# Kernel tuning notes

Hardware: AMD Instinct MI355X
Metric: run time of the kernel (lower is better)

## Reference

```python
import jax, jax.numpy as jnp
import numpy as np

B, S, E, H = 4, 1024, 256, 12  # batch, seq, emb_dim, num_heads; per-head dim == E (module quirk)


def setup_inputs() -> dict:
    key = jax.random.key(0)
    ks = jax.random.split(key, 9)
    s = 0.02
    x = jax.random.normal(ks[0], (B, S, E), dtype=jnp.float32)
    # additive causal mask (the module's tril buffer is unused; mask arrives via attention_mask)
    causal = jnp.tril(jnp.ones((S, S), dtype=jnp.float32))
    attention_mask = ((1.0 - causal) * -10000.0)[None, None, :, :]
    Wq = jax.random.normal(ks[1], (E, E * H), dtype=jnp.float32) * s
    bq = jnp.zeros((E * H,), dtype=jnp.float32)
    Wk = jax.random.normal(ks[2], (E, E * H), dtype=jnp.float32) * s
    bk = jnp.zeros((E * H,), dtype=jnp.float32)
    Wv = jax.random.normal(ks[3], (E, E * H), dtype=jnp.float32) * s
    bv = jnp.zeros((E * H,), dtype=jnp.float32)
    Wfc = jax.random.normal(ks[4], (E * H, E), dtype=jnp.float32) * s
    bfc = jnp.zeros((E,), dtype=jnp.float32)
    return {"x": x, "attention_mask": attention_mask, "Wq": Wq, "bq": bq,
            "Wk": Wk, "bk": bk, "Wv": Wv, "bv": bv, "Wfc": Wfc, "bfc": bfc}


def _split_heads(t):
    # (B, S, H*E) -> (B, H, S, E)
    b, s, _ = t.shape
    return t.reshape(b, s, H, E).transpose(0, 2, 1, 3)


def reference(x, attention_mask, Wq, bq, Wk, bk, Wv, bv, Wfc, bfc):
    q = _split_heads(x @ Wq + bq)
    k = _split_heads(x @ Wk + bk)
    v = _split_heads(x @ Wv + bv)
    scale = 1.0 / jnp.sqrt(jnp.asarray(E, dtype=x.dtype))
    scores = jnp.einsum('bhqd,bhkd->bhqk', q, k) * scale + attention_mask
    probs = jax.nn.softmax(scores, axis=-1)  # dropout p=0 in eval reference
    ctx = jnp.einsum('bhqk,bhkd->bhqd', probs, v)
    merged = ctx.transpose(0, 2, 1, 3).reshape(x.shape[0], x.shape[1], H * E)
    return merged @ Wfc + bfc
```

## Files before the change

### kernel.cpp

```cpp
#include <hip/hip_runtime.h>

#define BATCH 4
#define SEQ   1024
#define EMB   256
#define NH    12
#define EH    3072
#define MROWS 4096

typedef __attribute__((ext_vector_type(8))) short bf16x8;
typedef __attribute__((ext_vector_type(4))) float f32x4;
typedef __attribute__((ext_vector_type(4))) short short4v;

__device__ __forceinline__ short f2bf(float f) {
  union { float f; unsigned u; } x; x.f = f;
  unsigned r = x.u + 0x7fffu + ((x.u >> 16) & 1u);
  return (short)(r >> 16);
}

__device__ __forceinline__ unsigned pack_trunc(float a, float b) {
  union { float f; unsigned u; } x, y;
  x.f = a; y.f = b;
  return (x.u >> 16) | (y.u & 0xffff0000u);
}

__device__ __forceinline__ void gload_lds16(const void* g, void* l) {
  __builtin_amdgcn_global_load_lds(
      (const __attribute__((address_space(1))) unsigned*)g,
      (__attribute__((address_space(3))) unsigned*)l, 16, 0, 0);
}

__global__ __launch_bounds__(256) void cast_x_kernel(const float* __restrict__ in,
                                                     short* __restrict__ out) {
  int i = (blockIdx.x * 256 + threadIdx.x) * 4;
  float4 v = *(const float4*)(in + i);
  short4v o;
  o[0] = f2bf(v.x); o[1] = f2bf(v.y); o[2] = f2bf(v.z); o[3] = f2bf(v.w);
  *(short4v*)(out + i) = o;
}

__global__ __launch_bounds__(256) void transpose_qkv_kernel(const float* __restrict__ Wq,
                                                            const float* __restrict__ Wk,
                                                            const float* __restrict__ Wv,
                                                            short* __restrict__ Wt) {
  __shared__ float tile[32][33];
  const float* W = blockIdx.z == 0 ? Wq : (blockIdx.z == 1 ? Wk : Wv);
  short* o = Wt + (size_t)blockIdx.z * EH * EMB;
  const int n0 = blockIdx.x * 32, k0 = blockIdx.y * 32;
  const int tx = threadIdx.x & 31, ty = threadIdx.x >> 5;
#pragma unroll
  for (int i = 0; i < 4; i++)
    tile[ty + 8 * i][tx] = W[(size_t)(k0 + ty + 8 * i) * EH + n0 + tx];
  __syncthreads();
#pragma unroll
  for (int i = 0; i < 4; i++) {
    int nr = ty + 8 * i;
    o[(size_t)(n0 + nr) * EMB + k0 + tx] = f2bf(tile[tx][nr]);
  }
}

__global__ __launch_bounds__(256) void transpose_cast_kernel(const float* __restrict__ W,
                                                             short* __restrict__ Wt,
                                                             int K, int N) {
  __shared__ float tile[32][33];
  const int n0 = blockIdx.x * 32, k0 = blockIdx.y * 32;
  const int tx = threadIdx.x & 31, ty = threadIdx.x >> 5;
#pragma unroll
  for (int i = 0; i < 4; i++)
    tile[ty + 8 * i][tx] = W[(size_t)(k0 + ty + 8 * i) * N + n0 + tx];
  __syncthreads();
#pragma unroll
  for (int i = 0; i < 4; i++) {
    int nr = ty + 8 * i;
    Wt[(size_t)(n0 + nr) * K + k0 + tx] = f2bf(tile[tx][nr]);
  }
}

__global__ __launch_bounds__(256) void qkv_gemm_kernel(const short* __restrict__ A,
                                                       const short* __restrict__ Bt,
                                                       const float* __restrict__ bq,
                                                       const float* __restrict__ bk,
                                                       const float* __restrict__ bv,
                                                       short* __restrict__ qout,
                                                       short* __restrict__ kout,
                                                       short* __restrict__ vout) {
  constexpr int BM = 128, BK = 64, K = EMB;
  __shared__ short As[2][BM * BK];
  __shared__ short Bs[2][BM * BK];
  const int tid = threadIdx.x;
  const int w = tid >> 6, lane = tid & 63;
  const int wm = w >> 1, wn = w & 1;
  const int l15 = lane & 15, l4 = lane >> 4;
  const int m0 = blockIdx.x * BM, n0 = blockIdx.y * BM;

  f32x4 acc[4][4] = {};

  int srow[4], scol[4];
#pragma unroll
  for (int i = 0; i < 4; i++) {
    const int idx = i * 256 + tid;
    const int row = idx >> 3, sp = idx & 7, sl = sp ^ (row & 7);
    srow[i] = row;
    scol[i] = sl * 8;
  }

#define QKV_STAGE(bu, k0)                                                        \
  {                                                                              \
    _Pragma("unroll") for (int i = 0; i < 4; i++) {                              \
      const int idx = i * 256 + tid;                                             \
      gload_lds16(A + (size_t)(m0 + srow[i]) * K + (k0) + scol[i],               \
                  (char*)&As[bu][0] + idx * 16);                                 \
      gload_lds16(Bt + (size_t)(n0 + srow[i]) * K + (k0) + scol[i],              \
                  (char*)&Bs[bu][0] + idx * 16);                                 \
    }                                                                            \
  }

  QKV_STAGE(0, 0);
  asm volatile("s_waitcnt vmcnt(0)" ::: "memory");
  __syncthreads();

  int bu = 0;
  for (int k0 = 0; k0 < K; k0 += BK) {
    if (k0 + BK < K) QKV_STAGE(bu ^ 1, k0 + BK);

#pragma unroll
    for (int kst = 0; kst < 2; kst++) {
      const int sp = (kst * 4 + l4) ^ (l15 & 7);
      bf16x8 af[4], bfr[4];
#pragma unroll
      for (int mt = 0; mt < 4; mt++)
        af[mt] = *(const bf16x8*)&As[bu][(wm * 64 + mt * 16 + l15) * 64 + sp * 8];
#pragma unroll
      for (int nt = 0; nt < 4; nt++)
        bfr[nt] = *(const bf16x8*)&Bs[bu][(wn * 64 + nt * 16 + l15) * 64 + sp * 8];
      __builtin_amdgcn_s_setprio(1);
#pragma unroll
      for (int mt = 0; mt < 4; mt++)
#pragma unroll
        for (int nt = 0; nt < 4; nt++)
          acc[mt][nt] = __builtin_amdgcn_mfma_f32_16x16x32_bf16(af[mt], bfr[nt], acc[mt][nt], 0, 0, 0);
      __builtin_amdgcn_s_setprio(0);
    }

    asm volatile("s_waitcnt vmcnt(0)" ::: "memory");
    __syncthreads();
    bu ^= 1;
  }

  const int region = n0 / 3072;
  const float* bias = region == 0 ? bq : (region == 1 ? bk : bv);
  const float kQScale = 0.09016844f;
#pragma unroll
  for (int nt = 0; nt < 4; nt++) {
    const int n = n0 + wn * 64 + nt * 16 + l15;
    const int col = n - region * 3072;
    const float bvv = bias[col];
#pragma unroll
    for (int mt = 0; mt < 4; mt++) {
      const int mrow = m0 + wm * 64 + mt * 16 + 4 * l4;
      f32x4 v = acc[mt][nt];
      if (region == 0) {
#pragma unroll
        for (int r = 0; r < 4; r++)
          qout[(size_t)(mrow + r) * EH + col] = f2bf((v[r] + bvv) * kQScale);
      } else if (region == 1) {
#pragma unroll
        for (int r = 0; r < 4; r++)
          kout[(size_t)(mrow + r) * EH + col] = f2bf(v[r] + bvv);
      } else {
        const int bb = mrow >> 10;
        const int s  = mrow & 1023;
        const int h  = col >> 8, d = col & 255;
        short4v o4;
        o4[0] = f2bf(v[0] + bvv); o4[1] = f2bf(v[1] + bvv);
        o4[2] = f2bf(v[2] + bvv); o4[3] = f2bf(v[3] + bvv);
        *(short4v*)&vout[((size_t)(bb * NH + h) * EMB + d) * SEQ + s] = o4;
      }
    }
  }
#undef QKV_STAGE
}

__global__ __launch_bounds__(256) void fc_partial_kernel(const short* __restrict__ A,
                                                         const short* __restrict__ Bt,
                                                         float* __restrict__ Pout,
                                                         int M, int N, int K) {
  constexpr int BM = 64, BK = 128, KSL = 768;
  __shared__ short As[2][BM * BK];
  __shared__ short Bs[2][BM * BK];
  const int tid = threadIdx.x;
  const int w = tid >> 6, lane = tid & 63;
  const int wm = w >> 1, wn = w & 1;
  const int l15 = lane & 15, l4 = lane >> 4;
  const int m0 = blockIdx.x * BM, n0 = blockIdx.y * BM;
  const int kbase = blockIdx.z * KSL;
  float* P = Pout + (size_t)blockIdx.z * M * N;

  f32x4 acc[2][2] = {};

  int srow[4], scol[4];
#pragma unroll
  for (int i = 0; i < 4; i++) {
    const int idx = i * 256 + tid;
    const int row = idx >> 4, sp = idx & 15, sl = sp ^ (row & 15);
    srow[i] = row;
    scol[i] = sl * 8;
  }

#define FC_STAGE(bu, k0)                                                         \
  {                                                                              \
    _Pragma("unroll") for (int i = 0; i < 4; i++) {                              \
      const int idx = i * 256 + tid;                                             \
      gload_lds16(A + (size_t)(m0 + srow[i]) * K + (k0) + scol[i],               \
                  (char*)&As[bu][0] + idx * 16);                                 \
      gload_lds16(Bt + (size_t)(n0 + srow[i]) * K + (k0) + scol[i],              \
                  (char*)&Bs[bu][0] + idx * 16);                                 \
    }                                                                            \
  }

  FC_STAGE(0, kbase);
  asm volatile("s_waitcnt vmcnt(0)" ::: "memory");
  __syncthreads();

  int bu = 0;
  for (int k0 = kbase; k0 < kbase + KSL; k0 += BK) {
    if (k0 + BK < kbase + KSL) FC_STAGE(bu ^ 1, k0 + BK);

#pragma unroll
    for (int kst = 0; kst < 4; kst++) {
      const int sp = (kst * 4 + l4) ^ l15;
      bf16x8 af[2], bfr[2];
#pragma unroll
      for (int mt = 0; mt < 2; mt++)
        af[mt] = *(const bf16x8*)&As[bu][(wm * 32 + mt * 16 + l15) * 128 + sp * 8];
#pragma unroll
      for (int nt = 0; nt < 2; nt++)
        bfr[nt] = *(const bf16x8*)&Bs[bu][(wn * 32 + nt * 16 + l15) * 128 + sp * 8];
      __builtin_amdgcn_s_setprio(1);
#pragma unroll
      for (int mt = 0; mt < 2; mt++)
#pragma unroll
        for (int nt = 0; nt < 2; nt++)
          acc[mt][nt] = __builtin_amdgcn_mfma_f32_16x16x32_bf16(af[mt], bfr[nt], acc[mt][nt], 0, 0, 0);
      __builtin_amdgcn_s_setprio(0);
    }

    asm volatile("s_waitcnt vmcnt(0)" ::: "memory");
    __syncthreads();
    bu ^= 1;
  }

#pragma unroll
  for (int nt = 0; nt < 2; nt++) {
    const int n = n0 + wn * 32 + nt * 16 + l15;
#pragma unroll
    for (int mt = 0; mt < 2; mt++) {
      const int mrow = m0 + wm * 32 + mt * 16 + 4 * l4;
      f32x4 v = acc[mt][nt];
#pragma unroll
      for (int r = 0; r < 4; r++)
        P[(size_t)(mrow + r) * N + n] = v[r];
    }
  }
#undef FC_STAGE
}

__global__ __launch_bounds__(256) void fc_reduce_kernel(const float* __restrict__ Pin,
                                                        const float* __restrict__ bias,
                                                        float* __restrict__ out) {
  const int i4 = (blockIdx.x * 256 + threadIdx.x) * 4;
  const int n = i4 & 255;
  float4 s = *(const float4*)(bias + n);
#pragma unroll
  for (int ks = 0; ks < 4; ks++) {
    float4 p = *(const float4*)(Pin + (size_t)ks * MROWS * EMB + i4);
    s.x += p.x; s.y += p.y; s.z += p.z; s.w += p.w;
  }
  *(float4*)(out + i4) = s;
}

__global__ __launch_bounds__(512) void attn_kernel(const short* __restrict__ Q,
                                                   const short* __restrict__ Kg,
                                                   const short* __restrict__ Vt,
                                                   short* __restrict__ Ctx) {
  __shared__ short Ks[2][8192];
  __shared__ short Vs[2][8192];
  __shared__ short Ps[8][512];
  const int tid = threadIdx.x, w = tid >> 6, lane = tid & 63;
  const int l15 = lane & 15, l4 = lane >> 4;
  const int bh = blockIdx.x, b = bh / NH, h = bh % NH;
  const int qt = (gridDim.y - 1) - blockIdx.y;
  const int q0 = qt * 128;
  const int qw0 = q0 + w * 16;
  const int ntiles = 4 * qt + 4;

  const float kMaskL2 = -14426.95f;
  const float kThrL2  = 11.5f;

  const short* Kbase = Kg + (size_t)b * SEQ * EH + h * EMB;
  const short* Vbase = Vt + (size_t)bh * EMB * SEQ;

  int koff[2], voff[2];
#pragma unroll
  for (int i = 0; i < 2; i++) {
    const int idx = i * 512 + tid;
    {
      const int kv = (idx >> 3) & 31, sp = idx & 7, sl = sp ^ (kv & 7);
      koff[i] = kv * EH + (idx >> 8) * 64 + sl * 8;
    }
    {
      const int dp = idx >> 3, sp = idx & 7, sl = sp ^ (dp & 7);
      voff[i] = (dp * 2 + (sl >> 2)) * SEQ + (sl & 3) * 8;
    }
  }

  bf16x8 qf[8];
  {
    const short* qp = Q + (size_t)(b * SEQ + qw0 + l15) * EH + h * EMB + 8 * l4;
#pragma unroll
    for (int kst = 0; kst < 8; kst++) qf[kst] = *(const bf16x8*)(qp + 32 * kst);
  }

#pragma unroll
  for (int i = 0; i < 2; i++) {
    const int idx = i * 512 + tid;
    gload_lds16(Kbase + koff[i], (char*)&Ks[0][0] + idx * 16);
    gload_lds16(Vbase + voff[i], (char*)&Vs[0][0] + idx * 16);
  }
  asm volatile("s_waitcnt vmcnt(0)" ::: "memory");
  __syncthreads();

  f32x4 o[16] = {};
  float mst = -1e30f, lst = 0.f;

  int bu = 0;
  for (int t = 0; t < ntiles; t++) {
    const int kv0 = t * 32;

    if (t + 1 < ntiles) {
      const short* kp = Kbase + (size_t)(kv0 + 32) * EH;
      const short* vp = Vbase + kv0 + 32;
#pragma unroll
      for (int i = 0; i < 2; i++) {
        const int idx = i * 512 + tid;
        gload_lds16(kp + koff[i], (char*)&Ks[bu ^ 1][0] + idx * 16);
        gload_lds16(vp + voff[i], (char*)&Vs[bu ^ 1][0] + idx * 16);
      }
    }

    if (kv0 <= qw0 + 15) {
      f32x4 sf[2] = {};
      __builtin_amdgcn_s_setprio(1);
#pragma unroll
      for (int nt = 0; nt < 2; nt++)
#pragma unroll
        for (int kst = 0; kst < 8; kst++) {
          const int sp = (((kst & 1) << 2) + l4) ^ (l15 & 7);
          bf16x8 kf = *(const bf16x8*)&Ks[bu][(kst >> 1) * 2048 + (nt * 16 + l15) * 64 + sp * 8];
          sf[nt] = __builtin_amdgcn_mfma_f32_16x16x32_bf16(kf, qf[kst], sf[nt], 0, 0, 0);
        }
      __builtin_amdgcn_s_setprio(0);

      const bool maskt = (kv0 + 31 > qw0);
      float sval[2][4];
      float mxl = -1e30f;
#pragma unroll
      for (int nt = 0; nt < 2; nt++)
#pragma unroll
        for (int r = 0; r < 4; r++) {
          float s = sf[nt][r];
          if (maskt) {
            const int kv = kv0 + nt * 16 + 4 * l4 + r;
            s += (kv > qw0 + l15) ? kMaskL2 : 0.0f;
          }
          sval[nt][r] = s;
          mxl = fmaxf(mxl, s);
        }
      float mx = fmaxf(mxl, __shfl_xor(mxl, 16));
      mx = fmaxf(mx, __shfl_xor(mx, 32));
      const bool skipt = __all(mx <= mst + kThrL2);
      float mref, fsc;
      if (skipt) {
        fsc = 1.0f;
        mref = mst;
      } else {
        float mnew = fmaxf(mst, mx);
        fsc = exp2f(mst - mnew);
        mst = mnew;
        mref = mnew;
      }
      float pp[2][4];
      float lsum = 0.f;
#pragma unroll
      for (int nt = 0; nt < 2; nt++)
#pragma unroll
        for (int r = 0; r < 4; r++) {
          float e = exp2f(sval[nt][r] - mref);
          pp[nt][r] = e;
          lsum += e;
        }
      lst = lst * fsc + lsum;

      if (!skipt) {
        float fv[4];
#pragma unroll
        for (int r = 0; r < 4; r++)
          fv[r] = __shfl(fsc, (lane & 48) + 4 * (lane >> 4) + r);
#pragma unroll
        for (int nt = 0; nt < 16; nt++) {
          o[nt][0] *= fv[0]; o[nt][1] *= fv[1];
          o[nt][2] *= fv[2]; o[nt][3] *= fv[3];
        }
      }

#pragma unroll
      for (int nt = 0; nt < 2; nt++) {
        uint2 pk;
        pk.x = pack_trunc(pp[nt][0], pp[nt][1]);
        pk.y = pack_trunc(pp[nt][2], pp[nt][3]);
        const int col0 = nt * 16 + 4 * l4;
        const int pseg = (col0 >> 3) ^ ((l15 >> 1) & 3);
        *(uint2*)&Ps[w][l15 * 32 + pseg * 8 + (col0 & 7)] = pk;
      }

      const int aseg = l4 ^ ((l15 >> 1) & 3);
      bf16x8 af = *(const bf16x8*)&Ps[w][l15 * 32 + aseg * 8];
      const int vsp = ((l15 & 1) * 4 + l4) ^ (l15 >> 1);
      __builtin_amdgcn_s_setprio(1);
#pragma unroll
      for (int nt = 0; nt < 16; nt++) {
        const int dp = nt * 8 + (l15 >> 1);
        bf16x8 vf = *(const bf16x8*)&Vs[bu][dp * 64 + vsp * 8];
        o[nt] = __builtin_amdgcn_mfma_f32_16x16x32_bf16(af, vf, o[nt], 0, 0, 0);
      }
      __builtin_amdgcn_s_setprio(0);
    }

    asm volatile("s_waitcnt vmcnt(0)" ::: "memory");
    __syncthreads();
    bu ^= 1;
  }

  lst += __shfl_xor(lst, 16);
  lst += __shfl_xor(lst, 32);
  const float inv = 1.f / lst;
  float invv[4];
#pragma unroll
  for (int r = 0; r < 4; r++)
    invv[r] = __shfl(inv, (lane & 48) + 4 * (lane >> 4) + r);

  const int mrow = b * SEQ + qw0 + 4 * l4;
#pragma unroll
  for (int nt = 0; nt < 16; nt++) {
    const int d = h * EMB + nt * 16 + l15;
#pragma unroll
    for (int r = 0; r < 4; r++)
      Ctx[(size_t)(mrow + r) * EH + d] = f2bf(o[nt][r] * invv[r]);
  }
}

extern "C" void kernel_launch(void* const* d_in, const int* in_sizes, int n_in,
                              void* d_out, int out_size, void* d_ws, size_t ws_size,
                              hipStream_t stream) {
  const float* x   = (const float*)d_in[0];
  const float* Wq  = (const float*)d_in[2];
  const float* bq  = (const float*)d_in[3];
  const float* Wk  = (const float*)d_in[4];
  const float* bk  = (const float*)d_in[5];
  const float* Wv  = (const float*)d_in[6];
  const float* bv  = (const float*)d_in[7];
  const float* Wfc = (const float*)d_in[8];
  const float* bfc = (const float*)d_in[9];
  float* out = (float*)d_out;

  short* ws    = (short*)d_ws;
  short* xb    = ws;
  short* wqkvt = xb + 1048576;
  short* wfct  = wqkvt + 3 * 786432;
  short* q     = wfct + 786432;
  short* k     = q + 12582912;
  short* vt    = k + 12582912;
  short* ctx   = vt + 12582912;
  float* fcp   = (float*)q;

  cast_x_kernel<<<1024, 256, 0, stream>>>(x, xb);
  transpose_qkv_kernel<<<dim3(EH / 32, EMB / 32, 3), 256, 0, stream>>>(Wq, Wk, Wv, wqkvt);
  transpose_cast_kernel<<<dim3(EMB / 32, EH / 32), 256, 0, stream>>>(Wfc, wfct, EH, EMB);

  qkv_gemm_kernel<<<dim3(MROWS / 128, 9216 / 128), 256, 0, stream>>>(
      xb, wqkvt, bq, bk, bv, q, k, vt);

  attn_kernel<<<dim3(BATCH * NH, SEQ / 128), 512, 0, stream>>>(q, k, vt, ctx);

  fc_partial_kernel<<<dim3(MROWS / 64, EMB / 64, 4), 256, 0, stream>>>(
      ctx, wfct, fcp, MROWS, EMB, EH);
  fc_reduce_kernel<<<(MROWS * EMB / 4) / 256, 256, 0, stream>>>(fcp, bfc, out);
}
```

Baseline: 144.8 us.

## Switch attention to 32x32x16 MFMA with 4 waves and register-shuffled P

The attention kernel now uses 4 waves of 32 query rows each, with 32x32x16 bf16 MFMAs for both QK^T and PV. The P tile goes through cross-half lane shuffles instead of an LDS round trip, and the per-row rescale no longer needs shuffles because each lane owns one query row. The QKV GEMM swaps MFMA operand order for the Q/K regions so each lane holds 4 consecutive columns, which lets it write vectorized short4 stores and float4 bias loads. The cost is a larger accumulator and Q-fragment register footprint, and fewer threads per block, which may lower occupancy.

```diff
diff --git a/kernel.cpp b/kernel.cpp
--- a/kernel.cpp
+++ b/kernel.cpp
@@ -9,6 +9,7 @@
 
 typedef __attribute__((ext_vector_type(8))) short bf16x8;
 typedef __attribute__((ext_vector_type(4))) float f32x4;
+typedef __attribute__((ext_vector_type(16))) float f32x16;
 typedef __attribute__((ext_vector_type(4))) short short4v;
 
 __device__ __forceinline__ short f2bf(float f) {
@@ -91,6 +92,8 @@
   const int wm = w >> 1, wn = w & 1;
   const int l15 = lane & 15, l4 = lane >> 4;
   const int m0 = blockIdx.x * BM, n0 = blockIdx.y * BM;
+  const int region = n0 / 3072;
+  const bool qk = (region < 2);
 
   f32x4 acc[4][4] = {};
 
@@ -133,11 +136,19 @@
       for (int nt = 0; nt < 4; nt++)
         bfr[nt] = *(const bf16x8*)&Bs[bu][(wn * 64 + nt * 16 + l15) * 64 + sp * 8];
       __builtin_amdgcn_s_setprio(1);
-#pragma unroll
-      for (int mt = 0; mt < 4; mt++)
-#pragma unroll
-        for (int nt = 0; nt < 4; nt++)
-          acc[mt][nt] = __builtin_amdgcn_mfma_f32_16x16x32_bf16(af[mt], bfr[nt], acc[mt][nt], 0, 0, 0);
+      if (qk) {
+#pragma unroll
+        for (int mt = 0; mt < 4; mt++)
+#pragma unroll
+          for (int nt = 0; nt < 4; nt++)
+            acc[mt][nt] = __builtin_amdgcn_mfma_f32_16x16x32_bf16(bfr[nt], af[mt], acc[mt][nt], 0, 0, 0);
+      } else {
+#pragma unroll
+        for (int mt = 0; mt < 4; mt++)
+#pragma unroll
+          for (int nt = 0; nt < 4; nt++)
+            acc[mt][nt] = __builtin_amdgcn_mfma_f32_16x16x32_bf16(af[mt], bfr[nt], acc[mt][nt], 0, 0, 0);
+      }
       __builtin_amdgcn_s_setprio(0);
     }
 
@@ -146,27 +157,37 @@
     bu ^= 1;
   }
 
-  const int region = n0 / 3072;
-  const float* bias = region == 0 ? bq : (region == 1 ? bk : bv);
   const float kQScale = 0.09016844f;
-#pragma unroll
-  for (int nt = 0; nt < 4; nt++) {
-    const int n = n0 + wn * 64 + nt * 16 + l15;
-    const int col = n - region * 3072;
-    const float bvv = bias[col];
-#pragma unroll
-    for (int mt = 0; mt < 4; mt++) {
-      const int mrow = m0 + wm * 64 + mt * 16 + 4 * l4;
-      f32x4 v = acc[mt][nt];
-      if (region == 0) {
-#pragma unroll
-        for (int r = 0; r < 4; r++)
-          qout[(size_t)(mrow + r) * EH + col] = f2bf((v[r] + bvv) * kQScale);
-      } else if (region == 1) {
-#pragma unroll
-        for (int r = 0; r < 4; r++)
-          kout[(size_t)(mrow + r) * EH + col] = f2bf(v[r] + bvv);
-      } else {
+  if (qk) {
+    short* C = region == 0 ? qout : kout;
+    const float* bias = region == 0 ? bq : bk;
+    const float sc = region == 0 ? kQScale : 1.0f;
+#pragma unroll
+    for (int nt = 0; nt < 4; nt++) {
+      const int coln0 = (n0 - region * 3072) + wn * 64 + nt * 16 + 4 * l4;
+      const float4 bv4 = *(const float4*)&bias[coln0];
+#pragma unroll
+      for (int mt = 0; mt < 4; mt++) {
+        const int m = m0 + wm * 64 + mt * 16 + l15;
+        f32x4 v = acc[mt][nt];
+        short4v o4;
+        o4[0] = f2bf((v[0] + bv4.x) * sc);
+        o4[1] = f2bf((v[1] + bv4.y) * sc);
+        o4[2] = f2bf((v[2] + bv4.z) * sc);
+        o4[3] = f2bf((v[3] + bv4.w) * sc);
+        *(short4v*)&C[(size_t)m * EH + coln0] = o4;
+      }
+    }
+  } else {
+#pragma unroll
+    for (int nt = 0; nt < 4; nt++) {
+      const int n = n0 + wn * 64 + nt * 16 + l15;
+      const int col = n - 2 * 3072;
+      const float bvv = bv[col];
+#pragma unroll
+      for (int mt = 0; mt < 4; mt++) {
+        const int mrow = m0 + wm * 64 + mt * 16 + 4 * l4;
+        f32x4 v = acc[mt][nt];
         const int bb = mrow >> 10;
         const int s  = mrow & 1023;
         const int h  = col >> 8, d = col & 255;
@@ -278,19 +299,19 @@
   *(float4*)(out + i4) = s;
 }
 
-__global__ __launch_bounds__(512) void attn_kernel(const short* __restrict__ Q,
+__global__ __launch_bounds__(256) void attn_kernel(const short* __restrict__ Q,
                                                    const short* __restrict__ Kg,
                                                    const short* __restrict__ Vt,
                                                    short* __restrict__ Ctx) {
   __shared__ short Ks[2][8192];
   __shared__ short Vs[2][8192];
-  __shared__ short Ps[8][512];
   const int tid = threadIdx.x, w = tid >> 6, lane = tid & 63;
-  const int l15 = lane & 15, l4 = lane >> 4;
+  const int l31 = lane & 31, l5 = lane >> 5, l1 = lane & 1;
   const int bh = blockIdx.x, b = bh / NH, h = bh % NH;
   const int qt = (gridDim.y - 1) - blockIdx.y;
   const int q0 = qt * 128;
-  const int qw0 = q0 + w * 16;
+  const int qw0 = q0 + w * 32;
+  const int qglob = qw0 + l31;
   const int ntiles = 4 * qt + 4;
 
   const float kMaskL2 = -14426.95f;
@@ -299,13 +320,14 @@
   const short* Kbase = Kg + (size_t)b * SEQ * EH + h * EMB;
   const short* Vbase = Vt + (size_t)bh * EMB * SEQ;
 
-  int koff[2], voff[2];
-#pragma unroll
-  for (int i = 0; i < 2; i++) {
-    const int idx = i * 512 + tid;
+  int koff[4], voff[4];
+#pragma unroll
+  for (int i = 0; i < 4; i++) {
+    const int idx = i * 256 + tid;
     {
-      const int kv = (idx >> 3) & 31, sp = idx & 7, sl = sp ^ (kv & 7);
-      koff[i] = kv * EH + (idx >> 8) * 64 + sl * 8;
+      const int kv = idx >> 5, sp = idx & 31;
+      const int sl = (sp & 24) | ((sp & 7) ^ (kv & 7));
+      koff[i] = kv * EH + sl * 8;
     }
     {
       const int dp = idx >> 3, sp = idx & 7, sl = sp ^ (dp & 7);
@@ -313,23 +335,23 @@
     }
   }
 
-  bf16x8 qf[8];
+  bf16x8 qf[16];
   {
-    const short* qp = Q + (size_t)(b * SEQ + qw0 + l15) * EH + h * EMB + 8 * l4;
-#pragma unroll
-    for (int kst = 0; kst < 8; kst++) qf[kst] = *(const bf16x8*)(qp + 32 * kst);
-  }
-
-#pragma unroll
-  for (int i = 0; i < 2; i++) {
-    const int idx = i * 512 + tid;
+    const short* qp = Q + (size_t)(b * SEQ + qglob) * EH + h * EMB + 8 * l5;
+#pragma unroll
+    for (int i = 0; i < 16; i++) qf[i] = *(const bf16x8*)(qp + 16 * i);
+  }
+
+#pragma unroll
+  for (int i = 0; i < 4; i++) {
+    const int idx = i * 256 + tid;
     gload_lds16(Kbase + koff[i], (char*)&Ks[0][0] + idx * 16);
     gload_lds16(Vbase + voff[i], (char*)&Vs[0][0] + idx * 16);
   }
   asm volatile("s_waitcnt vmcnt(0)" ::: "memory");
   __syncthreads();
 
-  f32x4 o[16] = {};
+  f32x16 o[8] = {};
   float mst = -1e30f, lst = 0.f;
 
   int bu = 0;
@@ -340,43 +362,41 @@
       const short* kp = Kbase + (size_t)(kv0 + 32) * EH;
       const short* vp = Vbase + kv0 + 32;
 #pragma unroll
-      for (int i = 0; i < 2; i++) {
-        const int idx = i * 512 + tid;
+      for (int i = 0; i < 4; i++) {
+        const int idx = i * 256 + tid;
         gload_lds16(kp + koff[i], (char*)&Ks[bu ^ 1][0] + idx * 16);
         gload_lds16(vp + voff[i], (char*)&Vs[bu ^ 1][0] + idx * 16);
       }
     }
 
-    if (kv0 <= qw0 + 15) {
-      f32x4 sf[2] = {};
+    if (kv0 <= qw0 + 31) {
+      f32x16 s = {};
       __builtin_amdgcn_s_setprio(1);
 #pragma unroll
-      for (int nt = 0; nt < 2; nt++)
-#pragma unroll
-        for (int kst = 0; kst < 8; kst++) {
-          const int sp = (((kst & 1) << 2) + l4) ^ (l15 & 7);
-          bf16x8 kf = *(const bf16x8*)&Ks[bu][(kst >> 1) * 2048 + (nt * 16 + l15) * 64 + sp * 8];
-          sf[nt] = __builtin_amdgcn_mfma_f32_16x16x32_bf16(kf, qf[kst], sf[nt], 0, 0, 0);
+      for (int dstep = 0; dstep < 16; dstep++) {
+        const int seg = dstep * 2 + l5;
+        const int phys = (seg & 24) | ((seg & 7) ^ (l31 & 7));
+        bf16x8 kf = *(const bf16x8*)&Ks[bu][l31 * 256 + phys * 8];
+        s = __builtin_amdgcn_mfma_f32_32x32x16_bf16(kf, qf[dstep], s, 0, 0, 0);
+      }
+      __builtin_amdgcn_s_setprio(0);
+
+      const bool maskt = (kv0 + 31 > qw0);
+      float sval[16];
+      float mxl = -1e30f;
+#pragma unroll
+      for (int g = 0; g < 4; g++)
+#pragma unroll
+        for (int r = 0; r < 4; r++) {
+          float v = s[4 * g + r];
+          if (maskt) {
+            const int kv = kv0 + 8 * g + 4 * l5 + r;
+            v += (kv > qglob) ? kMaskL2 : 0.0f;
+          }
+          sval[4 * g + r] = v;
+          mxl = fmaxf(mxl, v);
         }
-      __builtin_amdgcn_s_setprio(0);
-
-      const bool maskt = (kv0 + 31 > qw0);
-      float sval[2][4];
-      float mxl = -1e30f;
-#pragma unroll
-      for (int nt = 0; nt < 2; nt++)
-#pragma unroll
-        for (int r = 0; r < 4; r++) {
-          float s = sf[nt][r];
-          if (maskt) {
-            const int kv = kv0 + nt * 16 + 4 * l4 + r;
-            s += (kv > qw0 + l15) ? kMaskL2 : 0.0f;
-          }
-          sval[nt][r] = s;
-          mxl = fmaxf(mxl, s);
-        }
-      float mx = fmaxf(mxl, __shfl_xor(mxl, 16));
-      mx = fmaxf(mx, __shfl_xor(mx, 32));
+      float mx = fmaxf(mxl, __shfl_xor(mxl, 32));
       const bool skipt = __all(mx <= mst + kThrL2);
       float mref, fsc;
       if (skipt) {
@@ -388,49 +408,51 @@
         mst = mnew;
         mref = mnew;
       }
-      float pp[2][4];
+      float pp[16];
       float lsum = 0.f;
 #pragma unroll
-      for (int nt = 0; nt < 2; nt++)
-#pragma unroll
-        for (int r = 0; r < 4; r++) {
-          float e = exp2f(sval[nt][r] - mref);
-          pp[nt][r] = e;
-          lsum += e;
+      for (int j = 0; j < 16; j++) {
+        float e = exp2f(sval[j] - mref);
+        pp[j] = e;
+        lsum += e;
+      }
+      lst = lst * fsc + lsum;
+
+      if (!skipt) {
+#pragma unroll
+        for (int dt = 0; dt < 8; dt++)
+#pragma unroll
+          for (int j = 0; j < 16; j++) o[dt][j] *= fsc;
+      }
+
+      unsigned pk0a = pack_trunc(pp[0], pp[1]),   pk0b = pack_trunc(pp[2], pp[3]);
+      unsigned pk1a = pack_trunc(pp[4], pp[5]),   pk1b = pack_trunc(pp[6], pp[7]);
+      unsigned pk2a = pack_trunc(pp[8], pp[9]),   pk2b = pack_trunc(pp[10], pp[11]);
+      unsigned pk3a = pack_trunc(pp[12], pp[13]), pk3b = pack_trunc(pp[14], pp[15]);
+
+      __builtin_amdgcn_s_setprio(1);
+#pragma unroll
+      for (int ks = 0; ks < 2; ks++) {
+        const unsigned ownA = ks ? pk2a : pk0a, ownB = ks ? pk2b : pk0b;
+        const unsigned othA = ks ? pk3a : pk1a, othB = ks ? pk3b : pk1b;
+        const unsigned sendA = l5 ? ownA : othA;
+        const unsigned sendB = l5 ? ownB : othB;
+        const unsigned recvA = (unsigned)__shfl_xor((int)sendA, 32);
+        const unsigned recvB = (unsigned)__shfl_xor((int)sendB, 32);
+        union { unsigned u[4]; bf16x8 v; } bb;
+        bb.u[0] = l5 ? recvA : ownA;
+        bb.u[1] = l5 ? recvB : ownB;
+        bb.u[2] = l5 ? othA : recvA;
+        bb.u[3] = l5 ? othB : recvB;
+        const bf16x8 bfrag = bb.v;
+#pragma unroll
+        for (int dt = 0; dt < 8; dt++) {
+          const int dp = dt * 16 + (l31 >> 1);
+          const int sl = l1 * 4 + 2 * ks + l5;
+          const int phys = sl ^ (dp & 7);
+          bf16x8 vf = *(const bf16x8*)&Vs[bu][dp * 64 + phys * 8];
+          o[dt] = __builtin_amdgcn_mfma_f32_32x32x16_bf16(vf, bfrag, o[dt], 0, 0, 0);
         }
-      lst = lst * fsc + lsum;
-
-      if (!skipt) {
-        float fv[4];
-#pragma unroll
-        for (int r = 0; r < 4; r++)
-          fv[r] = __shfl(fsc, (lane & 48) + 4 * (lane >> 4) + r);
-#pragma unroll
-        for (int nt = 0; nt < 16; nt++) {
-          o[nt][0] *= fv[0]; o[nt][1] *= fv[1];
-          o[nt][2] *= fv[2]; o[nt][3] *= fv[3];
-        }
-      }
-
-#pragma unroll
-      for (int nt = 0; nt < 2; nt++) {
-        uint2 pk;
-        pk.x = pack_trunc(pp[nt][0], pp[nt][1]);
-        pk.y = pack_trunc(pp[nt][2], pp[nt][3]);
-        const int col0 = nt * 16 + 4 * l4;
-        const int pseg = (col0 >> 3) ^ ((l15 >> 1) & 3);
-        *(uint2*)&Ps[w][l15 * 32 + pseg * 8 + (col0 & 7)] = pk;
-      }
-
-      const int aseg = l4 ^ ((l15 >> 1) & 3);
-      bf16x8 af = *(const bf16x8*)&Ps[w][l15 * 32 + aseg * 8];
-      const int vsp = ((l15 & 1) * 4 + l4) ^ (l15 >> 1);
-      __builtin_amdgcn_s_setprio(1);
-#pragma unroll
-      for (int nt = 0; nt < 16; nt++) {
-        const int dp = nt * 8 + (l15 >> 1);
-        bf16x8 vf = *(const bf16x8*)&Vs[bu][dp * 64 + vsp * 8];
-        o[nt] = __builtin_amdgcn_mfma_f32_16x16x32_bf16(af, vf, o[nt], 0, 0, 0);
       }
       __builtin_amdgcn_s_setprio(0);
     }
@@ -440,22 +462,21 @@
     bu ^= 1;
   }
 
-  lst += __shfl_xor(lst, 16);
   lst += __shfl_xor(lst, 32);
   const float inv = 1.f / lst;
-  float invv[4];
-#pragma unroll
-  for (int r = 0; r < 4; r++)
-    invv[r] = __shfl(inv, (lane & 48) + 4 * (lane >> 4) + r);
-
-  const int mrow = b * SEQ + qw0 + 4 * l4;
-#pragma unroll
-  for (int nt = 0; nt < 16; nt++) {
-    const int d = h * EMB + nt * 16 + l15;
-#pragma unroll
-    for (int r = 0; r < 4; r++)
-      Ctx[(size_t)(mrow + r) * EH + d] = f2bf(o[nt][r] * invv[r]);
-  }
+  short* cp = Ctx + (size_t)(b * SEQ + qglob) * EH + h * EMB;
+#pragma unroll
+  for (int dt = 0; dt < 8; dt++)
+#pragma unroll
+    for (int g = 0; g < 4; g++) {
+      const int d = 32 * dt + 8 * g + 4 * l5;
+      short4v o4;
+      o4[0] = f2bf(o[dt][4 * g + 0] * inv);
+      o4[1] = f2bf(o[dt][4 * g + 1] * inv);
+      o4[2] = f2bf(o[dt][4 * g + 2] * inv);
+      o4[3] = f2bf(o[dt][4 * g + 3] * inv);
+      *(short4v*)&cp[d] = o4;
+    }
 }
 
 extern "C" void kernel_launch(void* const* d_in, const int* in_sizes, int n_in,
@@ -489,7 +510,7 @@
   qkv_gemm_kernel<<<dim3(MROWS / 128, 9216 / 128), 256, 0, stream>>>(
       xb, wqkvt, bq, bk, bv, q, k, vt);
 
-  attn_kernel<<<dim3(BATCH * NH, SEQ / 128), 512, 0, stream>>>(q, k, vt, ctx);
+  attn_kernel<<<dim3(BATCH * NH, SEQ / 128), 256, 0, stream>>>(q, k, vt, ctx);
 
   fc_partial_kernel<<<dim3(MROWS / 64, EMB / 64, 4), 256, 0, stream>>>(
       ctx, wfct, fcp, MROWS, EMB, EH);
```

Measured after the change: 161.2 us. 1.11x slower.
